# Kernel tuning notes

Measured on AMD Instinct MI355X. Metric: run time of the kernel, lower is better.

Reference implementation:

```python
import jax, jax.numpy as jnp
import numpy as np
from jax import lax

B, T, D = 2048, 300, 40
H = 64          # BasicLSTMCell num_units
D1 = 128        # dense1 units
OUT = 512       # out_dim (num speakers)
FORGET_BIAS = 1.0
BN_EPS = 1e-3   # tf.layers.BatchNormalization default


def setup_inputs() -> dict:
    key = jax.random.key(0)
    ks = jax.random.split(key, 10)
    X = jax.random.normal(ks[0], (B, T, D), dtype=jnp.float32)
    seq_length = jax.random.randint(ks[1], (B,), 1, T + 1).astype(jnp.int32)
    # BasicLSTMCell kernel: [input_dim + H, 4H], gate order i, j, f, o
    lstm_kernel = jax.random.normal(ks[2], (D + H, 4 * H), dtype=jnp.float32) * 0.08
    lstm_bias = jnp.zeros((4 * H,), dtype=jnp.float32)
    W1 = jax.random.normal(ks[3], (H, D1), dtype=jnp.float32) * 0.1
    b1 = jnp.zeros((D1,), dtype=jnp.float32)
    gamma = jnp.ones((D1,), dtype=jnp.float32)
    beta = jnp.zeros((D1,), dtype=jnp.float32)
    moving_mean = jnp.zeros((D1,), dtype=jnp.float32)
    moving_var = jnp.ones((D1,), dtype=jnp.float32)
    W2 = jax.random.normal(ks[4], (D1, OUT), dtype=jnp.float32) * 0.1
    b2 = jnp.zeros((OUT,), dtype=jnp.float32)
    return {"X": X, "seq_length": seq_length,
            "lstm_kernel": lstm_kernel, "lstm_bias": lstm_bias,
            "W1": W1, "b1": b1, "gamma": gamma, "beta": beta,
            "moving_mean": moving_mean, "moving_var": moving_var,
            "W2": W2, "b2": b2}


def reference(X, seq_length, lstm_kernel, lstm_bias, W1, b1, gamma, beta,
              moving_mean, moving_var, W2, b2):
    b = X.shape[0]
    c0 = jnp.zeros((b, H), dtype=X.dtype)
    h0 = jnp.zeros((b, H), dtype=X.dtype)

    def step(carry, x_t):
        c, h = carry
        z = jnp.concatenate([x_t, h], axis=1) @ lstm_kernel + lstm_bias
        i, j, f, o = jnp.split(z, 4, axis=1)
        new_c = c * jax.nn.sigmoid(f + FORGET_BIAS) + jax.nn.sigmoid(i) * jnp.tanh(j)
        new_h = jnp.tanh(new_c) * jax.nn.sigmoid(o)
        return (new_c, new_h), new_h

    _, outs = lax.scan(step, (c0, h0), jnp.swapaxes(X, 0, 1))  # [T, B, H]
    outs = jnp.swapaxes(outs, 0, 1)  # [B, T, H]

    # gather last valid timestep per sample
    idx = (seq_length - 1).astype(jnp.int32)
    final = jnp.take_along_axis(outs, idx[:, None, None], axis=1)[:, 0, :]  # [B, H]

    x = jax.nn.relu(final @ W1 + b1)
    # BatchNorm in inference mode (training=False): use moving statistics
    x = gamma * (x - moving_mean) * lax.rsqrt(moving_var + BN_EPS) + beta
    return jax.nn.softmax(x @ W2 + b2, axis=-1)
```

## Files before the change

### kernel.cpp

```cpp
#include <hip/hip_runtime.h>
#include <stdint.h>

#define TT 300
#define DD 40
#define SB 8
#define ABYTES (8 * 192 * 2)
#define WROW 224

typedef __attribute__((ext_vector_type(8))) short short8;
typedef __attribute__((ext_vector_type(4))) float f32x4;

__device__ __forceinline__ ushort f2bf(float f) {
  uint32_t b = __float_as_uint(f);
  b += 0x7FFFu + ((b >> 16) & 1u);
  return (ushort)(b >> 16);
}

__device__ __forceinline__ void bar() {
  asm volatile("s_waitcnt lgkmcnt(0)" ::: "memory");
  __builtin_amdgcn_s_barrier();
  asm volatile("" ::: "memory");
}

__device__ __forceinline__ int aswz(int row, int colh) {
  return ((row * 192 + colh) * 2) ^ (row << 4);
}

__global__ __launch_bounds__(512, 2) void lstm_mfma_kernel(
    const float* __restrict__ X, const int* __restrict__ seqlen,
    const float* __restrict__ Wk, const float* __restrict__ bias,
    float* __restrict__ hfin)
{
  __shared__ ushort shmem[64 * WROW];
  char* const Ab = reinterpret_cast<char*>(shmem);

  const int tid = threadIdx.x;
  const int wv = tid >> 6, lane = tid & 63;
  const int q = lane >> 4, n = lane & 15, m = n & 7, b = n >> 3;
  const int s0 = blockIdx.x * SB;

  short8 Bf[6][2];
  for (int c = 0; c < 4; ++c) {
    for (int i = tid; i < 64 * 192; i += 512) {
      int cc = i & 63, kp = i >> 6;
      int nb = cc & 15, nt = (cc >> 4) & 1, ws = cc >> 5;
      int g = nt + 2 * (nb >> 3);
      int uu = (2 * c + ws) * 8 + (nb & 7);
      int col = g * 64 + uu;
      ushort v = 0;
      if (kp < 40) {
        v = f2bf(Wk[kp * 256 + col]);
      } else if (kp < 42) {
        float bv = bias[col] + ((g == 2) ? 1.0f : 0.0f);
        ushort hi = f2bf(bv);
        v = (kp == 40) ? hi : f2bf(bv - __uint_as_float((uint32_t)hi << 16));
      } else if (kp >= 64) {
        v = f2bf(Wk[(40 + ((kp - 64) >> 1)) * 256 + col]);
      }
      shmem[cc * WROW + kp] = v;
    }
    __syncthreads();
    if ((wv >> 1) == c) {
      const int cbase = (wv & 1) * 32;
      #pragma unroll
      for (int kt = 0; kt < 6; ++kt) {
        #pragma unroll
        for (int nt = 0; nt < 2; ++nt)
          Bf[kt][nt] = *reinterpret_cast<const short8*>(
              &shmem[(cbase + nt * 16 + n) * WROW + kt * 32 + q * 8]);
      }
    }
    __syncthreads();
  }

  for (int i = tid; i < 3072; i += 512) shmem[i] = 0;
  __syncthreads();

  const int hi2 = q >> 1;
  const int u = wv * 8 + m;
  const int sl = (q & 1) * 4 + hi2 * 2 + b;
  const int len = seqlen[s0 + sl];
  int ml = seqlen[s0 + (lane & 7)];
  #pragma unroll
  for (int off = 1; off < 8; off <<= 1) ml = max(ml, __shfl_xor(ml, off));

  const bool hasX = (tid < SB * DD);
  const int sA = (tid * 205) >> 13, dA = tid - sA * 40;
  const float* pA = X + (size_t)(s0 + sA) * (TT * DD) + dA;
  const int xb = aswz(sA, dA);

  if (tid < 16) {
    int s = tid & 7, bb = tid >> 3;
    *reinterpret_cast<uint32_t*>(Ab + bb * ABYTES + aswz(s, 40)) = 0x3F803F80u;
  }
  float xv = 0.f;
  if (hasX) {
    *reinterpret_cast<ushort*>(Ab + xb) = f2bf(pA[0]);
    if (ml > 1) xv = pA[DD];
  }
  __syncthreads();
  pA += 2 * DD;

  int aoff[6];
  #pragma unroll
  for (int kt = 0; kt < 6; ++kt)
    aoff[kt] = (m * 384 + kt * 64 + q * 16) ^ (m << 4);

  float cst = 0.f, hf = 0.f;
  float xvl = xv;
  const int hb = aswz(sl, 64 + 2 * u);
  const f32x4 zero4 = {0.f, 0.f, 0.f, 0.f};

  auto STEP = [&](int t, int RB, int WB) {
    short8 Ax0 = *reinterpret_cast<const short8*>(Ab + RB + aoff[0]);
    short8 Ax1 = *reinterpret_cast<const short8*>(Ab + RB + aoff[1]);
    short8 Ah0 = *reinterpret_cast<const short8*>(Ab + RB + aoff[2]);
    short8 Ah1 = *reinterpret_cast<const short8*>(Ab + RB + aoff[3]);
    short8 Ah2 = *reinterpret_cast<const short8*>(Ab + RB + aoff[4]);
    short8 Ah3 = *reinterpret_cast<const short8*>(Ab + RB + aoff[5]);

    f32x4 ac0 = __builtin_amdgcn_mfma_f32_16x16x32_bf16(Ax0, Bf[0][0], zero4, 0, 0, 0);
    f32x4 ac1 = __builtin_amdgcn_mfma_f32_16x16x32_bf16(Ax0, Bf[0][1], zero4, 0, 0, 0);
    ac0 = __builtin_amdgcn_mfma_f32_16x16x32_bf16(Ax1, Bf[1][0], ac0, 0, 0, 0);
    ac1 = __builtin_amdgcn_mfma_f32_16x16x32_bf16(Ax1, Bf[1][1], ac1, 0, 0, 0);

    if (hasX && t + 1 < ml) *reinterpret_cast<ushort*>(Ab + WB + xb) = f2bf(xvl);
    float xn = 0.f;
    if (hasX && t + 2 < ml) { xn = pA[0]; pA += DD; }

    ac0 = __builtin_amdgcn_mfma_f32_16x16x32_bf16(Ah0, Bf[2][0], ac0, 0, 0, 0);
    ac1 = __builtin_amdgcn_mfma_f32_16x16x32_bf16(Ah0, Bf[2][1], ac1, 0, 0, 0);
    ac0 = __builtin_amdgcn_mfma_f32_16x16x32_bf16(Ah1, Bf[3][0], ac0, 0, 0, 0);
    ac1 = __builtin_amdgcn_mfma_f32_16x16x32_bf16(Ah1, Bf[3][1], ac1, 0, 0, 0);
    ac0 = __builtin_amdgcn_mfma_f32_16x16x32_bf16(Ah2, Bf[4][0], ac0, 0, 0, 0);
    ac1 = __builtin_amdgcn_mfma_f32_16x16x32_bf16(Ah2, Bf[4][1], ac1, 0, 0, 0);
    ac0 = __builtin_amdgcn_mfma_f32_16x16x32_bf16(Ah3, Bf[5][0], ac0, 0, 0, 0);
    ac1 = __builtin_amdgcn_mfma_f32_16x16x32_bf16(Ah3, Bf[5][1], ac1, 0, 0, 0);

    float v0_s0 = hi2 ? ac0[2] : ac0[0];
    float v0_s1 = hi2 ? ac0[3] : ac0[1];
    float v1_s0 = hi2 ? ac1[2] : ac1[0];
    float v1_s1 = hi2 ? ac1[3] : ac1[1];
    float own0 = b ? v0_s1 : v0_s0;
    float own1 = b ? v1_s1 : v1_s0;
    float snd0 = b ? v0_s0 : v0_s1;
    float snd1 = b ? v1_s0 : v1_s1;
    float rcv0 = __shfl_xor(snd0, 8);
    float rcv1 = __shfl_xor(snd1, 8);
    float gi = b ? rcv0 : own0;
    float gj = b ? rcv1 : own1;
    float gf = b ? own0 : rcv0;
    float go = b ? own1 : rcv1;

    float Ef = __expf(-gf), Ei = __expf(-gi), Ej = __expf(2.f * gj);
    float nc = fmaf(cst, __builtin_amdgcn_rcpf(1.f + Ef),
                    (Ej - 1.f) * __builtin_amdgcn_rcpf((1.f + Ei) * (1.f + Ej)));
    float En = __expf(2.f * fminf(nc, 44.f)), Eo = __expf(-go);
    float nh = (En - 1.f) * __builtin_amdgcn_rcpf((1.f + En) * (1.f + Eo));
    cst = nc;
    if (t == len - 1) hf = nh;

    ushort hh = (ushort)(__float_as_uint(nh) >> 16);
    float rem = nh - __uint_as_float((uint32_t)hh << 16);
    ushort hl = (ushort)(__float_as_uint(rem) >> 16);
    *reinterpret_cast<uint32_t*>(Ab + WB + hb) = (uint32_t)hh | ((uint32_t)hl << 16);

    bar();
    xvl = xn;
  };

  for (int t = 0; t < ml; ) {
    STEP(t, 0, ABYTES); ++t;
    if (t >= ml) break;
    STEP(t, ABYTES, 0); ++t;
  }

  hfin[(size_t)(s0 + sl) * 64 + u] = hf;
}

__global__ __launch_bounds__(256, 1) void head_kernel(
    const float* __restrict__ hfin,
    const float* __restrict__ W1, const float* __restrict__ b1,
    const float* __restrict__ gamma, const float* __restrict__ beta,
    const float* __restrict__ mmean, const float* __restrict__ mvar,
    const float* __restrict__ W2, const float* __restrict__ b2,
    float* __restrict__ out)
{
  __shared__ float hl[16 * 64];
  __shared__ float d1t[128 * 20];
  __shared__ float lg[16 * 516];
  const int tid = threadIdx.x;
  const int b0 = blockIdx.x * 16;

  for (int i = tid; i < 16 * 64; i += 256) hl[i] = hfin[(size_t)b0 * 64 + i];
  __syncthreads();

  {
    const int j = tid & 127, sg = tid >> 7;
    float acc[8];
    const float bb = b1[j];
    #pragma unroll
    for (int s = 0; s < 8; ++s) acc[s] = bb;
    for (int k = 0; k < 64; ++k) {
      float w = W1[k * 128 + j];
      #pragma unroll
      for (int s = 0; s < 8; ++s) acc[s] = fmaf(hl[(sg * 8 + s) * 64 + k], w, acc[s]);
    }
    const float ga = gamma[j], be = beta[j], mm = mmean[j];
    const float iv = rsqrtf(mvar[j] + 1e-3f);
    #pragma unroll
    for (int s = 0; s < 8; ++s) {
      float v = fmaxf(acc[s], 0.f);
      d1t[j * 20 + sg * 8 + s] = ga * (v - mm) * iv + be;
    }
  }
  __syncthreads();

  {
    const int cA = tid * 2;
    float accA[16], accB[16];
    const float bA = b2[cA], bB = b2[cA + 1];
    #pragma unroll
    for (int s = 0; s < 16; ++s) { accA[s] = bA; accB[s] = bB; }
    for (int k = 0; k < 128; ++k) {
      const float2 w = *reinterpret_cast<const float2*>(&W2[k * 512 + cA]);
      const f32x4 dq0 = *reinterpret_cast<const f32x4*>(&d1t[k * 20]);
      const f32x4 dq1 = *reinterpret_cast<const f32x4*>(&d1t[k * 20 + 4]);
      const f32x4 dq2 = *reinterpret_cast<const f32x4*>(&d1t[k * 20 + 8]);
      const f32x4 dq3 = *reinterpret_cast<const f32x4*>(&d1t[k * 20 + 12]);
      #pragma unroll
      for (int s = 0; s < 4; ++s) {
        accA[s]      = fmaf(dq0[s], w.x, accA[s]);      accB[s]      = fmaf(dq0[s], w.y, accB[s]);
        accA[s + 4]  = fmaf(dq1[s], w.x, accA[s + 4]);  accB[s + 4]  = fmaf(dq1[s], w.y, accB[s + 4]);
        accA[s + 8]  = fmaf(dq2[s], w.x, accA[s + 8]);  accB[s + 8]  = fmaf(dq2[s], w.y, accB[s + 8]);
        accA[s + 12] = fmaf(dq3[s], w.x, accA[s + 12]); accB[s + 12] = fmaf(dq3[s], w.y, accB[s + 12]);
      }
    }
    #pragma unroll
    for (int s = 0; s < 16; ++s) {
      lg[s * 516 + cA]     = accA[s];
      lg[s * 516 + cA + 1] = accB[s];
    }
  }
  __syncthreads();

  {
    const int w = tid >> 6, lane = tid & 63;
    #pragma unroll
    for (int si = 0; si < 4; ++si) {
      const int s = w * 4 + si;
      float v[8];
      float mx = -3.4e38f;
      #pragma unroll
      for (int i = 0; i < 8; ++i) { v[i] = lg[s * 516 + lane + 64 * i]; mx = fmaxf(mx, v[i]); }
      #pragma unroll
      for (int off = 1; off < 64; off <<= 1) mx = fmaxf(mx, __shfl_xor(mx, off));
      float sum = 0.f;
      #pragma unroll
      for (int i = 0; i < 8; ++i) { v[i] = __expf(v[i] - mx); sum += v[i]; }
      #pragma unroll
      for (int off = 1; off < 64; off <<= 1) sum += __shfl_xor(sum, off);
      const float inv = __builtin_amdgcn_rcpf(sum);
      #pragma unroll
      for (int i = 0; i < 8; ++i)
        out[(size_t)(b0 + s) * 512 + lane + 64 * i] = v[i] * inv;
    }
  }
}

extern "C" void kernel_launch(void* const* d_in, const int* in_sizes, int n_in,
                              void* d_out, int out_size, void* d_ws, size_t ws_size,
                              hipStream_t stream) {
  const float* X      = (const float*)d_in[0];
  const int*   seqlen = (const int*)d_in[1];
  const float* Wk     = (const float*)d_in[2];
  const float* bias   = (const float*)d_in[3];
  const float* W1     = (const float*)d_in[4];
  const float* b1     = (const float*)d_in[5];
  const float* gam    = (const float*)d_in[6];
  const float* bet    = (const float*)d_in[7];
  const float* mmean  = (const float*)d_in[8];
  const float* mvar   = (const float*)d_in[9];
  const float* W2     = (const float*)d_in[10];
  const float* b2     = (const float*)d_in[11];
  float* out  = (float*)d_out;
  float* hfin = (float*)d_ws;

  lstm_mfma_kernel<<<dim3(2048 / SB), dim3(512), 0, stream>>>(X, seqlen, Wk, bias, hfin);
  head_kernel<<<dim3(128), dim3(256), 0, stream>>>(hfin, W1, b1, gam, bet,
                                                   mmean, mvar, W2, b2, out);
}
```

Baseline: 350.7 us.

## Switch LSTM recurrence MFMA from split-bf16 to single fp16 operands

Replaces bf16 operands, where h was carried as a hi/lo bf16 pair (K=192, 6 MFMA k-tiles), with plain fp16 for x, h and weights, cutting the K dimension to 128 (4 k-tiles). This removes two MFMA pairs and two LDS vector loads per timestep on the serial critical path and shrinks the A buffer. Weights are now converted directly into registers instead of staged through shared memory, which simplifies setup. It trades precision: h loses the extra low-order correction and fp16 has fewer exponent bits, which could affect accuracy over 300 recurrent steps.

After: 373.0 us. 1.06x slower.

```diff
diff --git a/kernel.cpp b/kernel.cpp
--- a/kernel.cpp
+++ b/kernel.cpp
@@ -4,17 +4,10 @@
 #define TT 300
 #define DD 40
 #define SB 8
-#define ABYTES (8 * 192 * 2)
-#define WROW 224
-
-typedef __attribute__((ext_vector_type(8))) short short8;
+#define ABYTES (8 * 128 * 2)
+
+typedef __attribute__((ext_vector_type(8))) _Float16 half8;
 typedef __attribute__((ext_vector_type(4))) float f32x4;
-
-__device__ __forceinline__ ushort f2bf(float f) {
-  uint32_t b = __float_as_uint(f);
-  b += 0x7FFFu + ((b >> 16) & 1u);
-  return (ushort)(b >> 16);
-}
 
 __device__ __forceinline__ void bar() {
   asm volatile("s_waitcnt lgkmcnt(0)" ::: "memory");
@@ -23,7 +16,7 @@
 }
 
 __device__ __forceinline__ int aswz(int row, int colh) {
-  return ((row * 192 + colh) * 2) ^ (row << 4);
+  return (row * 256 + colh * 2) ^ (row << 4);
 }
 
 __global__ __launch_bounds__(512, 2) void lstm_mfma_kernel(
@@ -31,50 +24,40 @@
     const float* __restrict__ Wk, const float* __restrict__ bias,
     float* __restrict__ hfin)
 {
-  __shared__ ushort shmem[64 * WROW];
-  char* const Ab = reinterpret_cast<char*>(shmem);
+  __shared__ char Ab[2 * ABYTES];
 
   const int tid = threadIdx.x;
   const int wv = tid >> 6, lane = tid & 63;
   const int q = lane >> 4, n = lane & 15, m = n & 7, b = n >> 3;
   const int s0 = blockIdx.x * SB;
 
-  short8 Bf[6][2];
-  for (int c = 0; c < 4; ++c) {
-    for (int i = tid; i < 64 * 192; i += 512) {
-      int cc = i & 63, kp = i >> 6;
-      int nb = cc & 15, nt = (cc >> 4) & 1, ws = cc >> 5;
-      int g = nt + 2 * (nb >> 3);
-      int uu = (2 * c + ws) * 8 + (nb & 7);
-      int col = g * 64 + uu;
-      ushort v = 0;
-      if (kp < 40) {
-        v = f2bf(Wk[kp * 256 + col]);
-      } else if (kp < 42) {
-        float bv = bias[col] + ((g == 2) ? 1.0f : 0.0f);
-        ushort hi = f2bf(bv);
-        v = (kp == 40) ? hi : f2bf(bv - __uint_as_float((uint32_t)hi << 16));
-      } else if (kp >= 64) {
-        v = f2bf(Wk[(40 + ((kp - 64) >> 1)) * 256 + col]);
+  for (int i = tid; i < 2 * ABYTES / 4; i += 512)
+    reinterpret_cast<uint32_t*>(Ab)[i] = 0;
+
+  half8 Bf[4][2];
+  #pragma unroll
+  for (int nt = 0; nt < 2; ++nt) {
+    const int g = nt + 2 * b;
+    const int col = g * 64 + 8 * wv + m;
+    const float bv = bias[col] + ((g == 2) ? 1.0f : 0.0f);
+    const _Float16 bhi = (_Float16)bv;
+    const _Float16 blo = (_Float16)(bv - (float)bhi);
+    #pragma unroll
+    for (int kt = 0; kt < 4; ++kt) {
+      half8 f;
+      #pragma unroll
+      for (int j = 0; j < 8; ++j) {
+        const int k = kt * 32 + q * 8 + j;
+        _Float16 v = (_Float16)0.f;
+        if (k < 40)       v = (_Float16)Wk[k * 256 + col];
+        else if (k == 40) v = bhi;
+        else if (k == 41) v = blo;
+        else if (k >= 64) v = (_Float16)Wk[(k - 24) * 256 + col];
+        f[j] = v;
       }
-      shmem[cc * WROW + kp] = v;
-    }
-    __syncthreads();
-    if ((wv >> 1) == c) {
-      const int cbase = (wv & 1) * 32;
-      #pragma unroll
-      for (int kt = 0; kt < 6; ++kt) {
-        #pragma unroll
-        for (int nt = 0; nt < 2; ++nt)
-          Bf[kt][nt] = *reinterpret_cast<const short8*>(
-              &shmem[(cbase + nt * 16 + n) * WROW + kt * 32 + q * 8]);
-      }
-    }
-    __syncthreads();
-  }
-
-  for (int i = tid; i < 3072; i += 512) shmem[i] = 0;
-  __syncthreads();
+      Bf[kt][nt] = f;
+    }
+  }
 
   const int hi2 = q >> 1;
   const int u = wv * 8 + m;
@@ -89,53 +72,47 @@
   const float* pA = X + (size_t)(s0 + sA) * (TT * DD) + dA;
   const int xb = aswz(sA, dA);
 
+  __syncthreads();
   if (tid < 16) {
     int s = tid & 7, bb = tid >> 3;
-    *reinterpret_cast<uint32_t*>(Ab + bb * ABYTES + aswz(s, 40)) = 0x3F803F80u;
-  }
-  float xv = 0.f;
+    *reinterpret_cast<uint32_t*>(Ab + bb * ABYTES + aswz(s, 40)) = 0x3C003C00u;
+  }
+  float xvl = 0.f;
   if (hasX) {
-    *reinterpret_cast<ushort*>(Ab + xb) = f2bf(pA[0]);
-    if (ml > 1) xv = pA[DD];
+    *reinterpret_cast<_Float16*>(Ab + xb) = (_Float16)pA[0];
+    if (ml > 1) xvl = pA[DD];
   }
   __syncthreads();
   pA += 2 * DD;
 
-  int aoff[6];
+  int aoff[4];
   #pragma unroll
-  for (int kt = 0; kt < 6; ++kt)
-    aoff[kt] = (m * 384 + kt * 64 + q * 16) ^ (m << 4);
+  for (int kt = 0; kt < 4; ++kt)
+    aoff[kt] = (m * 256 + kt * 64 + q * 16) ^ (m << 4);
 
   float cst = 0.f, hf = 0.f;
-  float xvl = xv;
-  const int hb = aswz(sl, 64 + 2 * u);
+  const int hb = aswz(sl, 64 + u);
   const f32x4 zero4 = {0.f, 0.f, 0.f, 0.f};
 
   auto STEP = [&](int t, int RB, int WB) {
-    short8 Ax0 = *reinterpret_cast<const short8*>(Ab + RB + aoff[0]);
-    short8 Ax1 = *reinterpret_cast<const short8*>(Ab + RB + aoff[1]);
-    short8 Ah0 = *reinterpret_cast<const short8*>(Ab + RB + aoff[2]);
-    short8 Ah1 = *reinterpret_cast<const short8*>(Ab + RB + aoff[3]);
-    short8 Ah2 = *reinterpret_cast<const short8*>(Ab + RB + aoff[4]);
-    short8 Ah3 = *reinterpret_cast<const short8*>(Ab + RB + aoff[5]);
-
-    f32x4 ac0 = __builtin_amdgcn_mfma_f32_16x16x32_bf16(Ax0, Bf[0][0], zero4, 0, 0, 0);
-    f32x4 ac1 = __builtin_amdgcn_mfma_f32_16x16x32_bf16(Ax0, Bf[0][1], zero4, 0, 0, 0);
-    ac0 = __builtin_amdgcn_mfma_f32_16x16x32_bf16(Ax1, Bf[1][0], ac0, 0, 0, 0);
-    ac1 = __builtin_amdgcn_mfma_f32_16x16x32_bf16(Ax1, Bf[1][1], ac1, 0, 0, 0);
-
-    if (hasX && t + 1 < ml) *reinterpret_cast<ushort*>(Ab + WB + xb) = f2bf(xvl);
+    half8 A0 = *reinterpret_cast<const half8*>(Ab + RB + aoff[0]);
+    half8 A1 = *reinterpret_cast<const half8*>(Ab + RB + aoff[1]);
+    half8 A2 = *reinterpret_cast<const half8*>(Ab + RB + aoff[2]);
+    half8 A3 = *reinterpret_cast<const half8*>(Ab + RB + aoff[3]);
+
+    f32x4 ac0 = __builtin_amdgcn_mfma_f32_16x16x32_f16(A0, Bf[0][0], zero4, 0, 0, 0);
+    f32x4 ac1 = __builtin_amdgcn_mfma_f32_16x16x32_f16(A0, Bf[0][1], zero4, 0, 0, 0);
+    ac0 = __builtin_amdgcn_mfma_f32_16x16x32_f16(A1, Bf[1][0], ac0, 0, 0, 0);
+    ac1 = __builtin_amdgcn_mfma_f32_16x16x32_f16(A1, Bf[1][1], ac1, 0, 0, 0);
+
+    if (hasX && t + 1 < ml) *reinterpret_cast<_Float16*>(Ab + WB + xb) = (_Float16)xvl;
     float xn = 0.f;
     if (hasX && t + 2 < ml) { xn = pA[0]; pA += DD; }
 
-    ac0 = __builtin_amdgcn_mfma_f32_16x16x32_bf16(Ah0, Bf[2][0], ac0, 0, 0, 0);
-    ac1 = __builtin_amdgcn_mfma_f32_16x16x32_bf16(Ah0, Bf[2][1], ac1, 0, 0, 0);
-    ac0 = __builtin_amdgcn_mfma_f32_16x16x32_bf16(Ah1, Bf[3][0], ac0, 0, 0, 0);
-    ac1 = __builtin_amdgcn_mfma_f32_16x16x32_bf16(Ah1, Bf[3][1], ac1, 0, 0, 0);
-    ac0 = __builtin_amdgcn_mfma_f32_16x16x32_bf16(Ah2, Bf[4][0], ac0, 0, 0, 0);
-    ac1 = __builtin_amdgcn_mfma_f32_16x16x32_bf16(Ah2, Bf[4][1], ac1, 0, 0, 0);
-    ac0 = __builtin_amdgcn_mfma_f32_16x16x32_bf16(Ah3, Bf[5][0], ac0, 0, 0, 0);
-    ac1 = __builtin_amdgcn_mfma_f32_16x16x32_bf16(Ah3, Bf[5][1], ac1, 0, 0, 0);
+    ac0 = __builtin_amdgcn_mfma_f32_16x16x32_f16(A2, Bf[2][0], ac0, 0, 0, 0);
+    ac1 = __builtin_amdgcn_mfma_f32_16x16x32_f16(A2, Bf[2][1], ac1, 0, 0, 0);
+    ac0 = __builtin_amdgcn_mfma_f32_16x16x32_f16(A3, Bf[3][0], ac0, 0, 0, 0);
+    ac1 = __builtin_amdgcn_mfma_f32_16x16x32_f16(A3, Bf[3][1], ac1, 0, 0, 0);
 
     float v0_s0 = hi2 ? ac0[2] : ac0[0];
     float v0_s1 = hi2 ? ac0[3] : ac0[1];
@@ -160,10 +137,7 @@
     cst = nc;
     if (t == len - 1) hf = nh;
 
-    ushort hh = (ushort)(__float_as_uint(nh) >> 16);
-    float rem = nh - __uint_as_float((uint32_t)hh << 16);
-    ushort hl = (ushort)(__float_as_uint(rem) >> 16);
-    *reinterpret_cast<uint32_t*>(Ab + WB + hb) = (uint32_t)hh | ((uint32_t)hl << 16);
+    *reinterpret_cast<_Float16*>(Ab + WB + hb) = (_Float16)nh;
 
     bar();
     xvl = xn;
```
